# Kernel tuning notes

Hardware: AMD Instinct MI355X
Metric: run time of the kernel (lower is better)

## Reference

```python
import jax, jax.numpy as jnp
import numpy as np

B, K, C = 64, 40, 1          # batch, num capsules, image channels
TH, TW = 16, 16              # template size
H, W = 96, 96                # output size
EPS_LOG = 1e-16              # safe_log epsilon


def setup_inputs() -> dict:
    key = jax.random.key(0)
    k1, k2, k3 = jax.random.split(key, 3)
    ident = jnp.array([1., 0., 0., 0., 1., 0.], dtype=jnp.float32)
    poses = ident + 0.1 * jax.random.normal(k1, (B, K, 6), dtype=jnp.float32)
    presences = jax.random.uniform(k2, (B, K), dtype=jnp.float32)
    templates = jax.random.normal(k3, (K, C, TH, TW), dtype=jnp.float32)
    return dict(poses=poses, presences=presences, templates=templates,
                bg_value=jnp.zeros((1,), jnp.float32),
                temperature_logit=jnp.zeros((1,), jnp.float32))


def reference(poses, presences, templates, bg_value, temperature_logit):
    # --- affine_grid (align_corners=False, PyTorch default) ---
    theta = poses.reshape(B * K, 2, 3)
    xs = (2.0 * jnp.arange(W, dtype=jnp.float32) + 1.0) / W - 1.0
    ys = (2.0 * jnp.arange(H, dtype=jnp.float32) + 1.0) / H - 1.0
    gx, gy = jnp.meshgrid(xs, ys)                       # [H,W]
    base = jnp.stack([gx, gy, jnp.ones_like(gx)], -1)   # [H,W,3]
    grid = jnp.einsum('nij,hwj->nhwi', theta, base).reshape(B, K, H, W, 2)

    # template nonlinearity
    templ = jax.nn.sigmoid(templates)                   # [K,C,TH,TW]

    # --- grid_sample bilinear, padding zeros, align_corners=False ---
    ix = ((grid[..., 0] + 1.0) * TW - 1.0) * 0.5        # [B,K,H,W]
    iy = ((grid[..., 1] + 1.0) * TH - 1.0) * 0.5
    x0 = jnp.floor(ix).astype(jnp.int32); x1 = x0 + 1
    y0 = jnp.floor(iy).astype(jnp.int32); y1 = y0 + 1
    wx1 = ix - x0.astype(ix.dtype); wx0 = 1.0 - wx1
    wy1 = iy - y0.astype(iy.dtype); wy0 = 1.0 - wy1
    kk = jnp.arange(K).reshape(1, K, 1, 1)

    def gather(y, x):
        v = templ[kk, :, jnp.clip(y, 0, TH - 1), jnp.clip(x, 0, TW - 1)]  # [B,K,H,W,C]
        inb = ((y >= 0) & (y < TH) & (x >= 0) & (x < TW))[..., None]
        return jnp.where(inb, v, 0.0)

    out = (gather(y0, x0) * (wy0 * wx0)[..., None]
           + gather(y0, x1) * (wy0 * wx1)[..., None]
           + gather(y1, x0) * (wy1 * wx0)[..., None]
           + gather(y1, x1) * (wy1 * wx1)[..., None])
    tt = jnp.moveaxis(out, -1, 2)                       # [B,K,C,H,W]

    # --- mixture postprocessing (no-alpha branch) ---
    temperature = jax.nn.softplus(temperature_logit + 0.5) + 1e-4   # (1,)
    pres = presences.reshape(B, K, 1, 1, 1)
    tt_logits = tt / temperature + jnp.log(jnp.clip(pres, EPS_LOG))
    bg = jax.nn.sigmoid(bg_value)                       # (1,)
    bg_image = jnp.broadcast_to(bg.reshape(1, 1, 1, 1, 1), (B, 1, C, H, W))
    bg_logits = bg_image / temperature                  # [B,1,C,H,W], C==1
    mixture_logits = jnp.concatenate([tt_logits, bg_logits], axis=1)  # [B,K+1,C,H,W]
    mixture_means = jnp.concatenate([tt, bg_image], axis=1)
    return jnp.stack([mixture_logits, mixture_means], 0)  # [2,B,K+1,C,H,W]
```

## Files before the change

### kernel.cpp

```cpp
#include <hip/hip_runtime.h>
#include <math.h>

#define NB 64
#define NK 40
#define TDIM 16
#define IMH 96
#define IMW 96
#define HW (IMH*IMW)
#define PLANES (NK+1)
#define PSTR 20
#define PROWS 19

__global__ __launch_bounds__(256) void TemplateImageDecoder_kernel(
    const float* __restrict__ poses,
    const float* __restrict__ presences,
    const float* __restrict__ templates,
    const float* __restrict__ bg_value,
    const float* __restrict__ temperature_logit,
    float* __restrict__ out)
{
    const int tid = threadIdx.x;
    const int bid = blockIdx.x;
    const int b = bid / PLANES;
    const int k = bid - b * PLANES;

    const float tl = temperature_logit[0] + 0.5f;
    const float sp = (tl > 0.0f) ? (tl + log1pf(expf(-tl))) : log1pf(expf(tl));
    const float invT = 1.0f / (sp + 1e-4f);

    const size_t plane = ((size_t)b * PLANES + k) * (size_t)HW;
    float4* __restrict__ outL4 = reinterpret_cast<float4*>(out + plane);
    float4* __restrict__ outM4 = reinterpret_cast<float4*>(out + (size_t)NB * PLANES * HW + plane);

    if (k == NK) {
        const float bg  = 1.0f / (1.0f + expf(-bg_value[0]));
        const float bgl = bg * invT;
        const float4 vl = {bgl, bgl, bgl, bgl};
        const float4 vm = {bg,  bg,  bg,  bg};
        #pragma unroll 3
        for (int it = 0; it < 9; ++it) {
            const int g = tid + it * 256;
            outL4[g] = vl;
            outM4[g] = vm;
        }
        return;
    }

    __shared__ float P[PROWS * PSTR];
    for (int i = tid; i < PROWS * PSTR; i += 256) P[i] = 0.0f;
    __syncthreads();
    {
        const float tv = templates[k * TDIM * TDIM + tid];
        const int y = tid >> 4, x = tid & 15;
        P[(y + 1) * PSTR + (x + 1)] = 1.0f / (1.0f + __expf(-tv));
    }

    const float* __restrict__ th = poses + ((size_t)b * NK + k) * 6;
    const float ax = 8.0f * th[0], bx_ = 8.0f * th[1], cx = fmaf(8.0f, th[2], 7.5f);
    const float ay = 8.0f * th[3], by_ = 8.0f * th[4], cy = fmaf(8.0f, th[5], 7.5f);
    const float sx = ax * (2.0f / IMW);
    const float sy = ay * (2.0f / IMW);
    const float p  = presences[b * NK + k];
    const float lp = logf(fmaxf(p, 1e-16f));
    __syncthreads();

    #pragma unroll 3
    for (int it = 0; it < 9; ++it) {
        const int g  = tid + it * 256;
        const int h  = g / (IMW / 4);
        const int w0 = (g - h * (IMW / 4)) * 4;
        const float gy  = (2.0f * h + 1.0f) * (1.0f / IMH) - 1.0f;
        const float gx0 = (2.0f * w0 + 1.0f) * (1.0f / IMW) - 1.0f;
        const float ix0 = fmaf(ax, gx0, fmaf(bx_, gy, cx));
        const float iy0 = fmaf(ay, gx0, fmaf(by_, gy, cy));
        float rM[4], rL[4];
        #pragma unroll
        for (int j = 0; j < 4; ++j) {
            float ix = fmaf((float)j, sx, ix0);
            float iy = fmaf((float)j, sy, iy0);
            ix = fminf(fmaxf(ix, -1.0f), 16.0f);
            iy = fminf(fmaxf(iy, -1.0f), 16.0f);
            const float x0f = floorf(ix), y0f = floorf(iy);
            const float fx = ix - x0f,   fy = iy - y0f;
            const int   x0 = (int)x0f,   y0 = (int)y0f;
            const int base = (y0 + 1) * PSTR + (x0 + 1);
            const float v00 = P[base],        v01 = P[base + 1];
            const float v10 = P[base + PSTR], v11 = P[base + PSTR + 1];
            const float wx0 = 1.0f - fx, wy0 = 1.0f - fy;
            const float top = fmaf(fx, v01, wx0 * v00);
            const float bot = fmaf(fx, v11, wx0 * v10);
            const float acc = fmaf(fy, bot, wy0 * top);
            rM[j] = acc;
            rL[j] = fmaf(acc, invT, lp);
        }
        outM4[g] = make_float4(rM[0], rM[1], rM[2], rM[3]);
        outL4[g] = make_float4(rL[0], rL[1], rL[2], rL[3]);
    }
}

extern "C" void kernel_launch(void* const* d_in, const int* in_sizes, int n_in,
                              void* d_out, int out_size, void* d_ws, size_t ws_size,
                              hipStream_t stream) {
    const float* poses             = (const float*)d_in[0];
    const float* presences         = (const float*)d_in[1];
    const float* templates         = (const float*)d_in[2];
    const float* bg_value          = (const float*)d_in[3];
    const float* temperature_logit = (const float*)d_in[4];
    float* out = (float*)d_out;

    TemplateImageDecoder_kernel<<<dim3(NB * PLANES), dim3(256), 0, stream>>>(
        poses, presences, templates, bg_value, temperature_logit, out);
}
```

Before: 36.68 us.

## Balance work across a fixed grid of blocks and use nontemporal stores

Replaces one-block-per-plane scheduling with a fixed grid of 2048 blocks. Each block processes an equal contiguous range of float4 output groups and may span plane boundaries, rebuilding the template tile in shared memory whenever it enters a new plane. Output writes become nontemporal stores, and launch bounds request 8 blocks per CU. The aim is to even out load between the cheap background planes and the sampled planes and to cut cache pollution from the write-heavy output, at the cost of extra per-segment setup and synchronisation.

```diff
diff --git a/kernel.cpp b/kernel.cpp
--- a/kernel.cpp
+++ b/kernel.cpp
@@ -10,8 +10,13 @@
 #define PLANES (NK+1)
 #define PSTR 20
 #define PROWS 19
+#define GPP (HW/4)
+#define NBLK 2048
+#define GPB ((NB*PLANES*GPP)/NBLK)
 
-__global__ __launch_bounds__(256) void TemplateImageDecoder_kernel(
+typedef float f32x4 __attribute__((ext_vector_type(4)));
+
+__global__ __launch_bounds__(256, 8) void TemplateImageDecoder_kernel(
     const float* __restrict__ poses,
     const float* __restrict__ presences,
     const float* __restrict__ templates,
@@ -21,80 +26,86 @@
 {
     const int tid = threadIdx.x;
     const int bid = blockIdx.x;
-    const int b = bid / PLANES;
-    const int k = bid - b * PLANES;
 
     const float tl = temperature_logit[0] + 0.5f;
     const float sp = (tl > 0.0f) ? (tl + log1pf(expf(-tl))) : log1pf(expf(tl));
     const float invT = 1.0f / (sp + 1e-4f);
 
-    const size_t plane = ((size_t)b * PLANES + k) * (size_t)HW;
-    float4* __restrict__ outL4 = reinterpret_cast<float4*>(out + plane);
-    float4* __restrict__ outM4 = reinterpret_cast<float4*>(out + (size_t)NB * PLANES * HW + plane);
-
-    if (k == NK) {
-        const float bg  = 1.0f / (1.0f + expf(-bg_value[0]));
-        const float bgl = bg * invT;
-        const float4 vl = {bgl, bgl, bgl, bgl};
-        const float4 vm = {bg,  bg,  bg,  bg};
-        #pragma unroll 3
-        for (int it = 0; it < 9; ++it) {
-            const int g = tid + it * 256;
-            outL4[g] = vl;
-            outM4[g] = vm;
-        }
-        return;
-    }
-
     __shared__ float P[PROWS * PSTR];
     for (int i = tid; i < PROWS * PSTR; i += 256) P[i] = 0.0f;
-    __syncthreads();
-    {
-        const float tv = templates[k * TDIM * TDIM + tid];
-        const int y = tid >> 4, x = tid & 15;
-        P[(y + 1) * PSTR + (x + 1)] = 1.0f / (1.0f + __expf(-tv));
-    }
 
-    const float* __restrict__ th = poses + ((size_t)b * NK + k) * 6;
-    const float ax = 8.0f * th[0], bx_ = 8.0f * th[1], cx = fmaf(8.0f, th[2], 7.5f);
-    const float ay = 8.0f * th[3], by_ = 8.0f * th[4], cy = fmaf(8.0f, th[5], 7.5f);
-    const float sx = ax * (2.0f / IMW);
-    const float sy = ay * (2.0f / IMW);
-    const float p  = presences[b * NK + k];
-    const float lp = logf(fmaxf(p, 1e-16f));
-    __syncthreads();
+    int s = bid * GPB;
+    const int e = s + GPB;
+    f32x4* __restrict__ outL_base = reinterpret_cast<f32x4*>(out);
+    f32x4* __restrict__ outM_base = reinterpret_cast<f32x4*>(out + (size_t)NB * PLANES * HW);
 
-    #pragma unroll 3
-    for (int it = 0; it < 9; ++it) {
-        const int g  = tid + it * 256;
-        const int h  = g / (IMW / 4);
-        const int w0 = (g - h * (IMW / 4)) * 4;
-        const float gy  = (2.0f * h + 1.0f) * (1.0f / IMH) - 1.0f;
-        const float gx0 = (2.0f * w0 + 1.0f) * (1.0f / IMW) - 1.0f;
-        const float ix0 = fmaf(ax, gx0, fmaf(bx_, gy, cx));
-        const float iy0 = fmaf(ay, gx0, fmaf(by_, gy, cy));
-        float rM[4], rL[4];
-        #pragma unroll
-        for (int j = 0; j < 4; ++j) {
-            float ix = fmaf((float)j, sx, ix0);
-            float iy = fmaf((float)j, sy, iy0);
-            ix = fminf(fmaxf(ix, -1.0f), 16.0f);
-            iy = fminf(fmaxf(iy, -1.0f), 16.0f);
-            const float x0f = floorf(ix), y0f = floorf(iy);
-            const float fx = ix - x0f,   fy = iy - y0f;
-            const int   x0 = (int)x0f,   y0 = (int)y0f;
-            const int base = (y0 + 1) * PSTR + (x0 + 1);
-            const float v00 = P[base],        v01 = P[base + 1];
-            const float v10 = P[base + PSTR], v11 = P[base + PSTR + 1];
-            const float wx0 = 1.0f - fx, wy0 = 1.0f - fy;
-            const float top = fmaf(fx, v01, wx0 * v00);
-            const float bot = fmaf(fx, v11, wx0 * v10);
-            const float acc = fmaf(fy, bot, wy0 * top);
-            rM[j] = acc;
-            rL[j] = fmaf(acc, invT, lp);
+    while (s < e) {
+        const int plane = s / GPP;
+        const int o = s - plane * GPP;
+        const int n = min(e - s, GPP - o);
+        const int b = plane / PLANES;
+        const int k = plane - b * PLANES;
+        f32x4* __restrict__ oL = outL_base + (size_t)plane * GPP;
+        f32x4* __restrict__ oM = outM_base + (size_t)plane * GPP;
+
+        if (k == NK) {
+            const float bg  = 1.0f / (1.0f + expf(-bg_value[0]));
+            const float bgl = bg * invT;
+            const f32x4 vl = {bgl, bgl, bgl, bgl};
+            const f32x4 vm = {bg,  bg,  bg,  bg};
+            for (int g = o + tid; g < o + n; g += 256) {
+                __builtin_nontemporal_store(vl, &oL[g]);
+                __builtin_nontemporal_store(vm, &oM[g]);
+            }
+        } else {
+            __syncthreads();
+            {
+                const float tv = templates[k * TDIM * TDIM + tid];
+                const int y = tid >> 4, x = tid & 15;
+                P[(y + 1) * PSTR + (x + 1)] = 1.0f / (1.0f + __expf(-tv));
+            }
+            const float* __restrict__ th = poses + ((size_t)b * NK + k) * 6;
+            const float ax = 8.0f * th[0], bx_ = 8.0f * th[1], cx = fmaf(8.0f, th[2], 7.5f);
+            const float ay = 8.0f * th[3], by_ = 8.0f * th[4], cy = fmaf(8.0f, th[5], 7.5f);
+            const float sx = ax * (2.0f / IMW);
+            const float sy = ay * (2.0f / IMW);
+            const float lp = logf(fmaxf(presences[b * NK + k], 1e-16f));
+            __syncthreads();
+
+            #pragma unroll 2
+            for (int g = o + tid; g < o + n; g += 256) {
+                const unsigned ug = (unsigned)g;
+                const int h  = ug / (IMW / 4);
+                const int w0 = (ug - h * (IMW / 4)) * 4;
+                const float gy  = (2.0f * h + 1.0f) * (1.0f / IMH) - 1.0f;
+                const float gx0 = (2.0f * w0 + 1.0f) * (1.0f / IMW) - 1.0f;
+                const float ix0 = fmaf(ax, gx0, fmaf(bx_, gy, cx));
+                const float iy0 = fmaf(ay, gx0, fmaf(by_, gy, cy));
+                f32x4 rM, rL;
+                #pragma unroll
+                for (int j = 0; j < 4; ++j) {
+                    float ix = fmaf((float)j, sx, ix0);
+                    float iy = fmaf((float)j, sy, iy0);
+                    ix = fminf(fmaxf(ix, -1.0f), 16.0f);
+                    iy = fminf(fmaxf(iy, -1.0f), 16.0f);
+                    const float x0f = floorf(ix), y0f = floorf(iy);
+                    const float fx = ix - x0f,   fy = iy - y0f;
+                    const int   x0 = (int)x0f,   y0 = (int)y0f;
+                    const int base = (y0 + 1) * PSTR + (x0 + 1);
+                    const float v00 = P[base],        v01 = P[base + 1];
+                    const float v10 = P[base + PSTR], v11 = P[base + PSTR + 1];
+                    const float wx0 = 1.0f - fx, wy0 = 1.0f - fy;
+                    const float top = fmaf(fx, v01, wx0 * v00);
+                    const float bot = fmaf(fx, v11, wx0 * v10);
+                    const float acc = fmaf(fy, bot, wy0 * top);
+                    rM[j] = acc;
+                    rL[j] = fmaf(acc, invT, lp);
+                }
+                __builtin_nontemporal_store(rM, &oM[g]);
+                __builtin_nontemporal_store(rL, &oL[g]);
+            }
         }
-        outM4[g] = make_float4(rM[0], rM[1], rM[2], rM[3]);
-        outL4[g] = make_float4(rL[0], rL[1], rL[2], rL[3]);
+        s += n;
     }
 }
 
@@ -108,6 +119,6 @@
     const float* temperature_logit = (const float*)d_in[4];
     float* out = (float*)d_out;
 
-    TemplateImageDecoder_kernel<<<dim3(NB * PLANES), dim3(256), 0, stream>>>(
+    TemplateImageDecoder_kernel<<<dim3(NBLK), dim3(256), 0, stream>>>(
         poses, presences, templates, bg_value, temperature_logit, out);
 }
```

After: 43.78 us. +19.3%, slower.
